# Kernel tuning notes

Hardware: AMD Instinct MI355X
Metric: run time of the kernel (lower is better)

Reference implementation:

```python
import jax, jax.numpy as jnp
import numpy as np

T = 16384
J = 21
IN = 3 * J + 278  # 341
H = 512
WIDTH = 64


def _gru_cell(x, h, w_ih, w_hh, b_ih, b_n):
    # equinox GRUCell math: igates = W_ih x + b; hgates = W_hh h
    ig = w_ih @ x + b_ih            # [3H]
    hg = w_hh @ h                   # [3H]
    ir, iz, inn = jnp.split(ig, 3)
    hr, hz, hn = jnp.split(hg, 3)
    r = jax.nn.sigmoid(ir + hr)
    z = jax.nn.sigmoid(iz + hz)
    n = jnp.tanh(inn + r * (hn + b_n))
    return n + z * (h - n)


def setup_inputs() -> dict:
    key = jax.random.key(0)
    ks = jax.random.split(key, 32)
    s = 0.02
    inp = {
        'dh_joint_pos_tj': jax.random.normal(ks[0], (T, J), jnp.float32),
        'dh_joint_vel_tj': jax.random.normal(ks[1], (T, J), jnp.float32),
        'com_inertia_tn': jax.random.normal(ks[2], (T, 160), jnp.float32),
        'com_vel_tn': jax.random.normal(ks[3], (T, 96), jnp.float32),
        'imu_acc_t3': jax.random.normal(ks[4], (T, 3), jnp.float32),
        'imu_gyro_t3': jax.random.normal(ks[5], (T, 3), jnp.float32),
        'act_frc_obs_tn': jax.random.normal(ks[6], (T, J), jnp.float32),
        'base_pos_t3': jax.random.normal(ks[7], (T, 3), jnp.float32),
        'base_quat_t4': jax.random.normal(ks[8], (T, 4), jnp.float32),
        'lin_vel_obs_t3': jax.random.normal(ks[9], (T, 3), jnp.float32),
        'ang_vel_obs_t3': jax.random.normal(ks[10], (T, 3), jnp.float32),
        'lin_vel_cmd_t2': jax.random.normal(ks[11], (T, 2), jnp.float32),
        'ang_vel_cmd_t1': jax.random.normal(ks[12], (T, 1), jnp.float32),
        'hidden_states_dn': jnp.zeros((2, H), jnp.float32),
        # GRU layer 0 (input IN -> H)
        'w_ih0': jax.random.normal(ks[13], (3 * H, IN), jnp.float32) * s,
        'w_hh0': jax.random.normal(ks[14], (3 * H, H), jnp.float32) * s,
        'b_ih0': jax.random.normal(ks[15], (3 * H,), jnp.float32) * s,
        'b_n0': jax.random.normal(ks[16], (H,), jnp.float32) * s,
        # GRU layer 1 (H -> H)
        'w_ih1': jax.random.normal(ks[17], (3 * H, H), jnp.float32) * s,
        'w_hh1': jax.random.normal(ks[18], (3 * H, H), jnp.float32) * s,
        'b_ih1': jax.random.normal(ks[19], (3 * H,), jnp.float32) * s,
        'b_n1': jax.random.normal(ks[20], (H,), jnp.float32) * s,
        # projector MLP: H -> 64 -> 64 -> 1, relu hidden activations
        'mw0': jax.random.normal(ks[21], (WIDTH, H), jnp.float32) * s,
        'mb0': jnp.zeros((WIDTH,), jnp.float32),
        'mw1': jax.random.normal(ks[22], (WIDTH, WIDTH), jnp.float32) * s,
        'mb1': jnp.zeros((WIDTH,), jnp.float32),
        'mw2': jax.random.normal(ks[23], (1, WIDTH), jnp.float32) * s,
        'mb2': jnp.zeros((1,), jnp.float32),
    }
    return inp


def reference(dh_joint_pos_tj, dh_joint_vel_tj, com_inertia_tn, com_vel_tn,
              imu_acc_t3, imu_gyro_t3, act_frc_obs_tn, base_pos_t3,
              base_quat_t4, lin_vel_obs_t3, ang_vel_obs_t3, lin_vel_cmd_t2,
              ang_vel_cmd_t1, hidden_states_dn,
              w_ih0, w_hh0, b_ih0, b_n0, w_ih1, w_hh1, b_ih1, b_n1,
              mw0, mb0, mw1, mb1, mw2, mb2):
    obs_tn = jnp.concatenate([
        dh_joint_pos_tj, dh_joint_vel_tj, com_inertia_tn, com_vel_tn,
        imu_acc_t3, imu_gyro_t3, act_frc_obs_tn, base_pos_t3, base_quat_t4,
        lin_vel_obs_t3, ang_vel_obs_t3, lin_vel_cmd_t2, ang_vel_cmd_t1,
    ], axis=-1)  # [T, 341]

    def scan_fn(carry, xt):
        h0 = _gru_cell(xt, carry[0], w_ih0, w_hh0, b_ih0, b_n0)
        h1 = _gru_cell(h0, carry[1], w_ih1, w_hh1, b_ih1, b_n1)
        v = jax.nn.relu(mw0 @ h1 + mb0)
        v = jax.nn.relu(mw1 @ v + mb1)
        yt = mw2 @ v + mb2  # [1]
        return jnp.stack([h0, h1], axis=0), yt

    new_hidden, out_tn = jax.lax.scan(scan_fn, hidden_states_dn, obs_tn)
    return out_tn, new_hidden
```

## Files before the change

kernel.cpp:

```cpp
#include <hip/hip_runtime.h>
#include <math.h>


#define T_STEPS 16384
#define IN_DIM 341
#define HID 512
#define G3 1536
#define TTILE 16
#define R0 2048
#define R0M (R0-1)
#define R1 8
#define R1M (R1-1)

__device__ __forceinline__ float dot4(float4 a, float4 b) {
  return fmaf(a.x, b.x, fmaf(a.y, b.y, fmaf(a.z, b.z, a.w * b.w)));
}
__device__ __forceinline__ float fast_sigmoid(float x) {
  return __builtin_amdgcn_rcpf(1.0f + __expf(-x));
}
__device__ __forceinline__ float fast_tanh(float x) {
  return fmaf(-2.0f, __builtin_amdgcn_rcpf(1.0f + __expf(2.0f * x)), 1.0f);
}
__device__ __forceinline__ unsigned long long ld_rlx64(const unsigned long long* p) {
  return __hip_atomic_load(p, __ATOMIC_RELAXED, __HIP_MEMORY_SCOPE_AGENT);
}
__device__ __forceinline__ void st_rlx64(unsigned long long* p, unsigned long long v) {
  __hip_atomic_store(p, v, __ATOMIC_RELAXED, __HIP_MEMORY_SCOPE_AGENT);
}
__device__ __forceinline__ unsigned ld_rlx32(const unsigned* p) {
  return __hip_atomic_load(p, __ATOMIC_RELAXED, __HIP_MEMORY_SCOPE_AGENT);
}
__device__ __forceinline__ void st_rlx32(unsigned* p, unsigned v) {
  __hip_atomic_store(p, v, __ATOMIC_RELAXED, __HIP_MEMORY_SCOPE_AGENT);
}
__device__ __forceinline__ unsigned long long pack_tv(unsigned tag, float v) {
  return ((unsigned long long)tag << 32) | (unsigned long long)__float_as_uint(v);
}
__device__ __forceinline__ float verify_ld(const unsigned long long* p, unsigned want) {
  unsigned long long w = ld_rlx64(p);
  while ((unsigned)(w >> 32) != want) {
    __builtin_amdgcn_s_sleep(1);
    w = ld_rlx64(p);
  }
  return __uint_as_float((unsigned)w);
}

__global__ __launch_bounds__(384) void concat_kernel(
    const float* __restrict__ p0, const float* __restrict__ p1,
    const float* __restrict__ p2, const float* __restrict__ p3,
    const float* __restrict__ p4, const float* __restrict__ p5,
    const float* __restrict__ p6, const float* __restrict__ p7,
    const float* __restrict__ p8, const float* __restrict__ p9,
    const float* __restrict__ p10, const float* __restrict__ p11,
    const float* __restrict__ p12, float* __restrict__ obs) {
  int t = blockIdx.x;
  int k = threadIdx.x;
  if (k >= IN_DIM) return;
  float v;
  if (k < 21)       v = p0[t*21 + k];
  else if (k < 42)  v = p1[t*21 + (k-21)];
  else if (k < 202) v = p2[t*160 + (k-42)];
  else if (k < 298) v = p3[t*96 + (k-202)];
  else if (k < 301) v = p4[t*3 + (k-298)];
  else if (k < 304) v = p5[t*3 + (k-301)];
  else if (k < 325) v = p6[t*21 + (k-304)];
  else if (k < 328) v = p7[t*3 + (k-325)];
  else if (k < 332) v = p8[t*4 + (k-328)];
  else if (k < 335) v = p9[t*3 + (k-332)];
  else if (k < 338) v = p10[t*3 + (k-335)];
  else if (k < 340) v = p11[t*2 + (k-338)];
  else              v = p12[t];
  obs[(size_t)t*IN_DIM + k] = v;
}

__global__ __launch_bounds__(256) void transpose_kernel(const float* __restrict__ w,
                                                        float* __restrict__ wT) {
  __shared__ float tile[32][33];
  int tx = threadIdx.x;
  int ty = threadIdx.y;
  int k = blockIdx.x*32 + tx;
#pragma unroll
  for (int jj = 0; jj < 4; jj++) {
    int r = blockIdx.y*32 + ty*4 + jj;
    tile[ty*4+jj][tx] = (k < IN_DIM) ? w[(size_t)r*IN_DIM + k] : 0.f;
  }
  __syncthreads();
#pragma unroll
  for (int jj = 0; jj < 4; jj++) {
    int kk = blockIdx.x*32 + ty*4 + jj;
    if (kk < IN_DIM) wT[(size_t)kk*G3 + blockIdx.y*32 + tx] = tile[tx][ty*4+jj];
  }
}

__global__ __launch_bounds__(256) void ig0_kernel(const float* __restrict__ wT,
                                                  const float* __restrict__ obs,
                                                  const float* __restrict__ b_ih0,
                                                  float* __restrict__ ig0) {
  int o = blockIdx.x*256 + threadIdx.x;
  int t0 = blockIdx.y * TTILE;
  float acc[TTILE];
  float b = b_ih0[o];
#pragma unroll
  for (int tt = 0; tt < TTILE; tt++) acc[tt] = b;
  for (int k = 0; k < IN_DIM; k++) {
    float wv = wT[(size_t)k*G3 + o];
#pragma unroll
    for (int tt = 0; tt < TTILE; tt++)
      acc[tt] = fmaf(obs[(size_t)(t0+tt)*IN_DIM + k], wv, acc[tt]);
  }
#pragma unroll
  for (int tt = 0; tt < TTILE; tt++)
    ig0[(size_t)(t0+tt)*G3 + o] = acc[tt];
}

__global__ __launch_bounds__(512) void init_kernel(const float* __restrict__ hid,
                                                   unsigned long long* ring0,
                                                   unsigned long long* ring1) {
  int e = threadIdx.x;
  st_rlx64(&ring0[e], pack_tv(0u, hid[e]));
  st_rlx64(&ring1[e], pack_tv(0u, hid[HID + e]));
}

__global__ __launch_bounds__(512, 2) void seq_kernel(
    const float* __restrict__ ig0, const float* __restrict__ w_hh0,
    const float* __restrict__ b_n0, const float* __restrict__ w_ih1,
    const float* __restrict__ w_hh1, const float* __restrict__ b_ih1,
    const float* __restrict__ b_n1,
    unsigned long long* ring0, unsigned long long* ring1, unsigned* cntB,
    float* __restrict__ h1a, float* __restrict__ d_out) {
  __shared__ float hbuf0[HID];
  __shared__ float hbuf1[HID];
  __shared__ float igbuf[96];
  const int tid = threadIdx.x;

  if ((int)blockIdx.x < 16) {
    const int wg = blockIdx.x;
    const int g  = tid >> 4;
    const int jj = tid & 15;
    const int eg = wg*32 + g;
    const bool leader = (jj == 0);
    float4 wr[8], wz[8], wn[8];
    {
      const float4* pr_ = (const float4*)(w_hh0 + (size_t)eg*HID);
      const float4* pz_ = (const float4*)(w_hh0 + (size_t)(512+eg)*HID);
      const float4* pn_ = (const float4*)(w_hh0 + (size_t)(1024+eg)*HID);
#pragma unroll
      for (int i = 0; i < 8; i++) {
        wr[i] = pr_[jj + 16*i]; wz[i] = pz_[jj + 16*i]; wn[i] = pn_[jj + 16*i];
      }
    }
    const float bn = b_n0[eg];
    for (int t = 0; t < T_STEPS; t++) {
      if ((t & 511) == 0 && t >= R0 && tid < 64) {
        const unsigned need = (unsigned)(t + 512 - R0);
        while (true) {
          unsigned v = ld_rlx32(&cntB[tid & 31]);
          if (__ballot(v >= need) == ~0ull) break;
          __builtin_amdgcn_s_sleep(16);
        }
      }
      if (tid < 96) {
        int gate = tid >> 5, e = tid & 31;
        igbuf[tid] = ig0[(size_t)t*G3 + gate*HID + wg*32 + e];
      }
      hbuf0[tid] = verify_ld(&ring0[(size_t)(t & R0M)*HID + tid], (unsigned)t);
      __syncthreads();
      float pr=0.f, pz=0.f, pn=0.f;
      const float4* hp = (const float4*)hbuf0;
#pragma unroll
      for (int i = 0; i < 8; i++) {
        float4 hv = hp[jj + 16*i];
        pr += dot4(wr[i],hv); pz += dot4(wz[i],hv); pn += dot4(wn[i],hv);
      }
#pragma unroll
      for (int s = 1; s < 16; s <<= 1) {
        pr += __shfl_xor(pr, s, 16);
        pz += __shfl_xor(pz, s, 16);
        pn += __shfl_xor(pn, s, 16);
      }
      if (leader) {
        float r = fast_sigmoid(igbuf[g] + pr);
        float z = fast_sigmoid(igbuf[32+g] + pz);
        float n = fast_tanh(igbuf[64+g] + r*(pn + bn));
        float hnew = n + z*(hbuf0[eg] - n);
        st_rlx64(&ring0[(size_t)((t+1) & R0M)*HID + eg],
                 pack_tv((unsigned)(t+1), hnew));
        if (t == T_STEPS-1) d_out[T_STEPS + eg] = hnew;
      }
      __syncthreads();
    }
  } else {
    const int wg  = (int)blockIdx.x - 16;
    const int g   = tid >> 5;
    const int j32 = tid & 31;
    const int half = j32 >> 4;
    const int jj  = j32 & 15;
    const int eg  = wg*16 + g;
    const bool leader = (j32 == 0);
    const float* Wm = half ? w_hh1 : w_ih1;
    float4 ar[8], az[8], an[8];
    {
      const float4* pr_ = (const float4*)(Wm + (size_t)eg*HID);
      const float4* pz_ = (const float4*)(Wm + (size_t)(512+eg)*HID);
      const float4* pn_ = (const float4*)(Wm + (size_t)(1024+eg)*HID);
#pragma unroll
      for (int i = 0; i < 8; i++) {
        ar[i] = pr_[jj + 16*i]; az[i] = pz_[jj + 16*i]; an[i] = pn_[jj + 16*i];
      }
    }
    const float cr = b_ih1[eg], cz = b_ih1[512+eg], cn = b_ih1[1024+eg];
    const float bnn = b_n1[eg];
    for (int t = 0; t < T_STEPS; t++) {
      hbuf0[tid] = verify_ld(&ring0[(size_t)((t+1) & R0M)*HID + tid], (unsigned)(t+1));
      hbuf1[tid] = verify_ld(&ring1[(size_t)(t & R1M)*HID + tid], (unsigned)t);
      __syncthreads();
      const float4* hp = (const float4*)(half ? hbuf1 : hbuf0);
      float pr=0.f, pz=0.f, pn=0.f;
#pragma unroll
      for (int i = 0; i < 8; i++) {
        float4 hv = hp[jj + 16*i];
        pr += dot4(ar[i],hv); pz += dot4(az[i],hv); pn += dot4(an[i],hv);
      }
#pragma unroll
      for (int s = 1; s < 16; s <<= 1) {
        pr += __shfl_xor(pr, s, 16);
        pz += __shfl_xor(pz, s, 16);
        pn += __shfl_xor(pn, s, 16);
      }
      float qr = __shfl(pr, 16, 32);
      float qz = __shfl(pz, 16, 32);
      float qn = __shfl(pn, 16, 32);
      if (leader) {
        float r = fast_sigmoid(pr + cr + qr);
        float z = fast_sigmoid(pz + cz + qz);
        float n = fast_tanh(pn + cn + r*(qn + bnn));
        float hnew = n + z*(hbuf1[eg] - n);
        st_rlx64(&ring1[(size_t)((t+1) & R1M)*HID + eg],
                 pack_tv((unsigned)(t+1), hnew));
        h1a[(size_t)t*HID + eg] = hnew;
        if (t == T_STEPS-1) d_out[T_STEPS + HID + eg] = hnew;
      }
      __syncthreads();
      if (tid == 0 && (t & 31) == 31)
        st_rlx32(&cntB[wg], (unsigned)(t+1));
    }
  }
}

__global__ __launch_bounds__(64) void mlp_kernel(
    const float* __restrict__ h1_all, const float* __restrict__ mw0,
    const float* __restrict__ mb0, const float* __restrict__ mw1,
    const float* __restrict__ mb1, const float* __restrict__ mw2,
    const float* __restrict__ mb2, float* __restrict__ out) {
  const int l = threadIdx.x;
  const int t0 = blockIdx.x * 8;
  __shared__ float v0s[8][64];
  float acc[8];
#pragma unroll
  for (int tt = 0; tt < 8; tt++) acc[tt] = mb0[l];
  const float4* w = (const float4*)(mw0 + (size_t)l*512);
#pragma unroll 4
  for (int i = 0; i < 128; i++) {
    float4 a = w[i];
#pragma unroll
    for (int tt = 0; tt < 8; tt++) {
      float4 b = ((const float4*)(h1_all + (size_t)(t0+tt)*512))[i];
      acc[tt] = fmaf(a.x,b.x, fmaf(a.y,b.y, fmaf(a.z,b.z, fmaf(a.w,b.w, acc[tt]))));
    }
  }
#pragma unroll
  for (int tt = 0; tt < 8; tt++) v0s[tt][l] = fmaxf(acc[tt], 0.f);
  __syncthreads();
  float acc1[8];
#pragma unroll
  for (int tt = 0; tt < 8; tt++) acc1[tt] = mb1[l];
  const float* w1 = mw1 + (size_t)l*64;
  for (int jj = 0; jj < 64; jj++) {
    float wv = w1[jj];
#pragma unroll
    for (int tt = 0; tt < 8; tt++) acc1[tt] = fmaf(wv, v0s[tt][jj], acc1[tt]);
  }
  float w2 = mw2[l];
  float bb = mb2[0];
#pragma unroll
  for (int tt = 0; tt < 8; tt++) {
    float y = w2 * fmaxf(acc1[tt], 0.f);
#pragma unroll
    for (int s = 32; s > 0; s >>= 1) y += __shfl_down(y, s, 64);
    if (l == 0) out[t0+tt] = y + bb;
  }
}

extern "C" void kernel_launch(void* const* d_in, const int* in_sizes, int n_in,
                              void* d_out, int out_size, void* d_ws, size_t ws_size,
                              hipStream_t stream) {
  const float* p0  = (const float*)d_in[0];
  const float* p1  = (const float*)d_in[1];
  const float* p2  = (const float*)d_in[2];
  const float* p3  = (const float*)d_in[3];
  const float* p4  = (const float*)d_in[4];
  const float* p5  = (const float*)d_in[5];
  const float* p6  = (const float*)d_in[6];
  const float* p7  = (const float*)d_in[7];
  const float* p8  = (const float*)d_in[8];
  const float* p9  = (const float*)d_in[9];
  const float* p10 = (const float*)d_in[10];
  const float* p11 = (const float*)d_in[11];
  const float* p12 = (const float*)d_in[12];
  const float* hid   = (const float*)d_in[13];
  const float* w_ih0 = (const float*)d_in[14];
  const float* w_hh0 = (const float*)d_in[15];
  const float* b_ih0 = (const float*)d_in[16];
  const float* b_n0  = (const float*)d_in[17];
  const float* w_ih1 = (const float*)d_in[18];
  const float* w_hh1 = (const float*)d_in[19];
  const float* b_ih1 = (const float*)d_in[20];
  const float* b_n1  = (const float*)d_in[21];
  const float* mw0 = (const float*)d_in[22];
  const float* mb0 = (const float*)d_in[23];
  const float* mw1 = (const float*)d_in[24];
  const float* mb1 = (const float*)d_in[25];
  const float* mw2 = (const float*)d_in[26];
  const float* mb2 = (const float*)d_in[27];
  float* out = (float*)d_out;

  char* base = (char*)d_ws;
  const size_t IG0_B = (size_t)T_STEPS*G3*4;
  const size_t R0_B  = (size_t)R0*HID*8;
  const size_t R1_B  = (size_t)R1*HID*8;
  const size_t CNT_B = 1024;
  const size_t H1A_B = (size_t)T_STEPS*HID*4;
  float* ig0 = (float*)base;
  unsigned long long* ring0 = (unsigned long long*)(base + IG0_B);
  unsigned long long* ring1 = (unsigned long long*)(base + IG0_B + R0_B);
  unsigned* cntB = (unsigned*)(base + IG0_B + R0_B + R1_B);
  float* h1a = (float*)(base + IG0_B + R0_B + R1_B + CNT_B);
  float* obs = h1a;
  float* wT  = (float*)((char*)h1a + (size_t)T_STEPS*IN_DIM*4);
  if (ws_size < IG0_B + R0_B + R1_B + CNT_B + H1A_B) return;

  hipMemsetAsync(cntB, 0, CNT_B, stream);
  concat_kernel<<<T_STEPS, 384, 0, stream>>>(p0,p1,p2,p3,p4,p5,p6,p7,p8,p9,p10,p11,p12, obs);
  transpose_kernel<<<dim3(11,48), dim3(32,8), 0, stream>>>(w_ih0, wT);
  ig0_kernel<<<dim3(6, T_STEPS/TTILE), 256, 0, stream>>>(wT, obs, b_ih0, ig0);
  init_kernel<<<1, 512, 0, stream>>>(hid, ring0, ring1);
  seq_kernel<<<48, 512, 0, stream>>>(ig0, w_hh0, b_n0, w_ih1, w_hh1, b_ih1, b_n1,
                                     ring0, ring1, cntB, h1a, out);
  mlp_kernel<<<T_STEPS/8, 64, 0, stream>>>(h1a, mw0, mb0, mw1, mb1, mw2, mb2, out);
}
```

Baseline: 31.85 ms.

## Double-buffer shared state to drop second barrier and prefetch input gates

Shared hidden-state and input-gate buffers become double-buffered by step parity, so the trailing __syncthreads in each recurrent step can go. The next step's input-gate values are prefetched into a register during the current step. Layer-1 blocks now issue both ring loads before spinning on either. Weight registers are pinned with empty asm, and launch bounds drop to one block per CU to allow more registers. The risk is subtle races, since a single barrier per step with parity buffers relies on the cross-block tag protocol to keep fast waves from overwriting data still being read.

```diff
diff --git a/kernel.cpp b/kernel.cpp
--- a/kernel.cpp
+++ b/kernel.cpp
@@ -35,6 +35,9 @@
 }
 __device__ __forceinline__ unsigned long long pack_tv(unsigned tag, float v) {
   return ((unsigned long long)tag << 32) | (unsigned long long)__float_as_uint(v);
+}
+__device__ __forceinline__ void pin4(float4& v) {
+  asm volatile("" : "+v"(v.x), "+v"(v.y), "+v"(v.z), "+v"(v.w));
 }
 __device__ __forceinline__ float verify_ld(const unsigned long long* p, unsigned want) {
   unsigned long long w = ld_rlx64(p);
@@ -121,16 +124,16 @@
   st_rlx64(&ring1[e], pack_tv(0u, hid[HID + e]));
 }
 
-__global__ __launch_bounds__(512, 2) void seq_kernel(
+__global__ __launch_bounds__(512, 1) void seq_kernel(
     const float* __restrict__ ig0, const float* __restrict__ w_hh0,
     const float* __restrict__ b_n0, const float* __restrict__ w_ih1,
     const float* __restrict__ w_hh1, const float* __restrict__ b_ih1,
     const float* __restrict__ b_n1,
     unsigned long long* ring0, unsigned long long* ring1, unsigned* cntB,
     float* __restrict__ h1a, float* __restrict__ d_out) {
-  __shared__ float hbuf0[HID];
-  __shared__ float hbuf1[HID];
-  __shared__ float igbuf[96];
+  __shared__ float hbuf0[2][HID];
+  __shared__ float hbuf1[2][HID];
+  __shared__ float igbuf[2][96];
   const int tid = threadIdx.x;
 
   if ((int)blockIdx.x < 16) {
@@ -139,6 +142,7 @@
     const int jj = tid & 15;
     const int eg = wg*32 + g;
     const bool leader = (jj == 0);
+    const int iggate = tid >> 5, ige = tid & 31;
     float4 wr[8], wz[8], wn[8];
     {
       const float4* pr_ = (const float4*)(w_hh0 + (size_t)eg*HID);
@@ -147,10 +151,18 @@
 #pragma unroll
       for (int i = 0; i < 8; i++) {
         wr[i] = pr_[jj + 16*i]; wz[i] = pz_[jj + 16*i]; wn[i] = pn_[jj + 16*i];
+        pin4(wr[i]); pin4(wz[i]); pin4(wn[i]);
       }
     }
     const float bn = b_n0[eg];
+    if (tid < 96) igbuf[0][tid] = ig0[(size_t)iggate*HID + wg*32 + ige];
     for (int t = 0; t < T_STEPS; t++) {
+      const int p = t & 1;
+      float igpre = 0.f;
+      if (tid < 96) {
+        int tn = (t+1 < T_STEPS) ? t+1 : t;
+        igpre = ig0[(size_t)tn*G3 + iggate*HID + wg*32 + ige];
+      }
       if ((t & 511) == 0 && t >= R0 && tid < 64) {
         const unsigned need = (unsigned)(t + 512 - R0);
         while (true) {
@@ -159,14 +171,10 @@
           __builtin_amdgcn_s_sleep(16);
         }
       }
-      if (tid < 96) {
-        int gate = tid >> 5, e = tid & 31;
-        igbuf[tid] = ig0[(size_t)t*G3 + gate*HID + wg*32 + e];
-      }
-      hbuf0[tid] = verify_ld(&ring0[(size_t)(t & R0M)*HID + tid], (unsigned)t);
+      hbuf0[p][tid] = verify_ld(&ring0[(size_t)(t & R0M)*HID + tid], (unsigned)t);
       __syncthreads();
       float pr=0.f, pz=0.f, pn=0.f;
-      const float4* hp = (const float4*)hbuf0;
+      const float4* hp = (const float4*)hbuf0[p];
 #pragma unroll
       for (int i = 0; i < 8; i++) {
         float4 hv = hp[jj + 16*i];
@@ -179,15 +187,15 @@
         pn += __shfl_xor(pn, s, 16);
       }
       if (leader) {
-        float r = fast_sigmoid(igbuf[g] + pr);
-        float z = fast_sigmoid(igbuf[32+g] + pz);
-        float n = fast_tanh(igbuf[64+g] + r*(pn + bn));
-        float hnew = n + z*(hbuf0[eg] - n);
+        float r = fast_sigmoid(igbuf[p][g] + pr);
+        float z = fast_sigmoid(igbuf[p][32+g] + pz);
+        float n = fast_tanh(igbuf[p][64+g] + r*(pn + bn));
+        float hnew = n + z*(hbuf0[p][eg] - n);
         st_rlx64(&ring0[(size_t)((t+1) & R0M)*HID + eg],
                  pack_tv((unsigned)(t+1), hnew));
         if (t == T_STEPS-1) d_out[T_STEPS + eg] = hnew;
       }
-      __syncthreads();
+      if (tid < 96) igbuf[p ^ 1][tid] = igpre;
     }
   } else {
     const int wg  = (int)blockIdx.x - 16;
@@ -206,15 +214,24 @@
 #pragma unroll
       for (int i = 0; i < 8; i++) {
         ar[i] = pr_[jj + 16*i]; az[i] = pz_[jj + 16*i]; an[i] = pn_[jj + 16*i];
+        pin4(ar[i]); pin4(az[i]); pin4(an[i]);
       }
     }
     const float cr = b_ih1[eg], cz = b_ih1[512+eg], cn = b_ih1[1024+eg];
     const float bnn = b_n1[eg];
     for (int t = 0; t < T_STEPS; t++) {
-      hbuf0[tid] = verify_ld(&ring0[(size_t)((t+1) & R0M)*HID + tid], (unsigned)(t+1));
-      hbuf1[tid] = verify_ld(&ring1[(size_t)(t & R1M)*HID + tid], (unsigned)t);
+      const int p = t & 1;
+      const unsigned long long* s0 = &ring0[(size_t)((t+1) & R0M)*HID + tid];
+      const unsigned long long* s1 = &ring1[(size_t)(t & R1M)*HID + tid];
+      const unsigned w0t = (unsigned)(t+1), w1t = (unsigned)t;
+      unsigned long long v0 = ld_rlx64(s0);
+      unsigned long long v1 = ld_rlx64(s1);
+      while ((unsigned)(v0 >> 32) != w0t) { __builtin_amdgcn_s_sleep(1); v0 = ld_rlx64(s0); }
+      while ((unsigned)(v1 >> 32) != w1t) { __builtin_amdgcn_s_sleep(1); v1 = ld_rlx64(s1); }
+      hbuf0[p][tid] = __uint_as_float((unsigned)v0);
+      hbuf1[p][tid] = __uint_as_float((unsigned)v1);
       __syncthreads();
-      const float4* hp = (const float4*)(half ? hbuf1 : hbuf0);
+      const float4* hp = (const float4*)(half ? hbuf1[p] : hbuf0[p]);
       float pr=0.f, pz=0.f, pn=0.f;
 #pragma unroll
       for (int i = 0; i < 8; i++) {
@@ -234,13 +251,12 @@
         float r = fast_sigmoid(pr + cr + qr);
         float z = fast_sigmoid(pz + cz + qz);
         float n = fast_tanh(pn + cn + r*(qn + bnn));
-        float hnew = n + z*(hbuf1[eg] - n);
+        float hnew = n + z*(hbuf1[p][eg] - n);
         st_rlx64(&ring1[(size_t)((t+1) & R1M)*HID + eg],
                  pack_tv((unsigned)(t+1), hnew));
         h1a[(size_t)t*HID + eg] = hnew;
         if (t == T_STEPS-1) d_out[T_STEPS + HID + eg] = hnew;
       }
-      __syncthreads();
       if (tid == 0 && (t & 31) == 31)
         st_rlx32(&cntB[wg], (unsigned)(t+1));
     }
```

Result: slower. 40.55 ms (+27.3%).
